# Optimization experiments

Hardware: AMD Instinct MI355X
Metric: run time of the kernel (lower is better)

The kernel has to match this reference:

```python
import jax, jax.numpy as jnp
import numpy as np

B, S, I, H = 128, 256, 512, 512


def setup_inputs() -> dict:
    key = jax.random.key(0)
    ks = jax.random.split(key, 7)
    scale = 1.0 / np.sqrt(H)
    return {
        "x": jax.random.normal(ks[0], (B, S, I), dtype=jnp.float32),
        "hx": jax.random.normal(ks[1], (B, H), dtype=jnp.float32),
        "mask": jax.random.uniform(ks[2], (B, S, 1), dtype=jnp.float32),
        # torch nn.GRUCell params: weight_ih [3H, I], weight_hh [3H, H], biases [3H]
        "W_ih": jax.random.uniform(ks[3], (3 * H, I), minval=-scale, maxval=scale, dtype=jnp.float32),
        "W_hh": jax.random.uniform(ks[4], (3 * H, H), minval=-scale, maxval=scale, dtype=jnp.float32),
        "b_ih": jax.random.uniform(ks[5], (3 * H,), minval=-scale, maxval=scale, dtype=jnp.float32),
        "b_hh": jax.random.uniform(ks[6], (3 * H,), minval=-scale, maxval=scale, dtype=jnp.float32),
    }


def reference(x, hx, mask, W_ih, W_hh, b_ih, b_hh):
    # Precompute input projections for all timesteps in one big GEMM: [B,S,3H]
    gi = jnp.einsum("bsi,gi->bsg", x, W_ih) + b_ih
    gi_s = jnp.moveaxis(gi, 1, 0)      # [S,B,3H]
    mask_s = jnp.moveaxis(mask, 1, 0)  # [S,B,1]

    def step(h, inp):
        gi_t, m_t = inp
        h = h * m_t                                    # masked reset of hidden state
        gh = h @ W_hh.T + b_hh                         # [B,3H]
        i_r, i_z, i_n = jnp.split(gi_t, 3, axis=-1)    # torch gate order: r, z, n
        h_r, h_z, h_n = jnp.split(gh, 3, axis=-1)
        r = jax.nn.sigmoid(i_r + h_r)
        z = jax.nn.sigmoid(i_z + h_z)
        n = jnp.tanh(i_n + r * h_n)
        h_new = (1.0 - z) * n + z * h
        return h_new, h_new

    h_last, hs = jax.lax.scan(step, hx, (gi_s, mask_s))
    return jnp.moveaxis(hs, 0, 1), h_last  # ([B,S,H], [B,H])
```

## Files before the change

kernel.cpp:

```cpp
#include <hip/hip_runtime.h>

typedef __attribute__((ext_vector_type(8))) short bf16x8;
typedef __attribute__((ext_vector_type(4))) float f32x4;
typedef unsigned short ushort_t;
typedef unsigned int uint32;
typedef unsigned long long u64;

#define DEVI __device__ __forceinline__

static constexpr int Bn = 128, Sn = 256, In = 512, Hn = 512;
static constexpr int G3 = 3 * Hn;
static constexpr int GBLK = 32;

static constexpr size_t GI_OFF    = 0;
static constexpr size_t GI_BYTES  = (size_t)Bn * Sn * G3 * 2;
static constexpr size_t WIH_OFF   = GI_OFF + GI_BYTES;
static constexpr size_t WIH_BYTES = (size_t)G3 * In * 2;
static constexpr size_t HBUF_OFF  = WIH_OFF + WIH_BYTES;
static constexpr size_t HBUF_BYTES= (size_t)2 * Bn * Hn * 2;
static constexpr size_t FLAG_OFF  = HBUF_OFF + HBUF_BYTES;
static constexpr size_t FLAG_BYTES= 4096;

DEVI ushort_t f2bf(float f) {
  uint32 u = __builtin_bit_cast(uint32, f);
  u += 0x7FFFu + ((u >> 16) & 1u);
  return (ushort_t)(u >> 16);
}
DEVI float bf2f(ushort_t h) {
  uint32 u = ((uint32)h) << 16;
  return __builtin_bit_cast(float, u);
}
DEVI float sigmoid_f(float x) { return 1.0f / (1.0f + __expf(-x)); }
DEVI float tanh_f(float x)    { return 2.0f / (1.0f + __expf(-2.0f * x)) - 1.0f; }

__global__ void k_cvt_wih(const float* __restrict__ wih, ushort_t* __restrict__ out) {
  int i = blockIdx.x * blockDim.x + threadIdx.x;
  const float4 v = ((const float4*)wih)[i];
  ushort4 o;
  o.x = f2bf(v.x); o.y = f2bf(v.y); o.z = f2bf(v.z); o.w = f2bf(v.w);
  ((ushort4*)out)[i] = o;
}

__launch_bounds__(512)
__global__ void k_gi(const float* __restrict__ x, const ushort_t* __restrict__ wihb,
                     const float* __restrict__ b_ih, ushort_t* __restrict__ gi) {
  extern __shared__ ushort_t apan[];
  const int tid = threadIdx.x;
  const int bm  = blockIdx.x;
#pragma unroll
  for (int it = 0; it < 32; ++it) {
    int fidx = it * 512 + tid;
    int row = fidx >> 7, c4 = fidx & 127;
    const float4 v = *(const float4*)(x + ((size_t)(bm * 128 + row) << 9) + (c4 << 2));
    ushort4 o;
    o.x = f2bf(v.x); o.y = f2bf(v.y); o.z = f2bf(v.z); o.w = f2bf(v.w);
    *(ushort4*)(&apan[row * 520 + (c4 << 2)]) = o;
  }
  __syncthreads();
  const int lane = tid & 63, wid = tid >> 6;
  const int l15 = lane & 15, hi = lane >> 4;
  const int arow = wid * 16 + l15;
  for (int nt = 0; nt < 12; ++nt) {
    const int n0 = nt * 128;
    f32x4 acc[8] = {};
#pragma unroll
    for (int ks = 0; ks < 16; ++ks) {
      bf16x8 a = *(const bf16x8*)(&apan[arow * 520 + ks * 32 + hi * 8]);
#pragma unroll
      for (int j = 0; j < 8; ++j) {
        const ushort_t* wp = wihb + ((size_t)(n0 + j * 16 + l15) << 9) + ks * 32 + hi * 8;
        bf16x8 b = *(const bf16x8*)wp;
        acc[j] = __builtin_amdgcn_mfma_f32_16x16x32_bf16(a, b, acc[j], 0, 0, 0);
      }
    }
#pragma unroll
    for (int j = 0; j < 8; ++j) {
      const int n = n0 + j * 16 + l15;
      const float bias = b_ih[n];
#pragma unroll
      for (int r = 0; r < 4; ++r) {
        int m = bm * 128 + wid * 16 + hi * 4 + r;
        gi[(size_t)m * 1536 + n] = f2bf(acc[j][r] + bias);
      }
    }
  }
}

__launch_bounds__(512)
__global__ void k_scan(const float* __restrict__ hx, const float* __restrict__ mask,
                       const float* __restrict__ whh, const float* __restrict__ bhh,
                       const ushort_t* __restrict__ gi, u64* __restrict__ hbuf,
                       uint32* __restrict__ flags, float* __restrict__ out) {
  __shared__ ushort_t Wl[48 * 520];
  __shared__ ushort_t hpack[128 * 16];
  __shared__ int s_abort;
  const int tid = threadIdx.x;
  const int bid = blockIdx.x;
  const int c0 = bid * 16;
  if (tid == 0) s_abort = 0;

  for (int r = 0; r < 48; ++r) {
    int g = r >> 4, j = r & 15;
    Wl[r * 520 + tid] = f2bf(whh[(size_t)(g * 512 + c0 + j) * 512 + tid]);
  }

  const int lane = tid & 63, wid = tid >> 6;
  const int l15 = lane & 15, hi = lane >> 4;
  const int arow = wid * 16 + l15;

  float hreg[4];
#pragma unroll
  for (int r = 0; r < 4; ++r) {
    int b = wid * 16 + hi * 4 + r;
    hreg[r] = hx[b * 512 + c0 + l15] * mask[b * 256];
    hpack[b * 16 + l15] = f2bf(hreg[r]);
  }
  __syncthreads();
  {
    int b = tid >> 2, q = tid & 3;
    u64 v = *(const u64*)(&hpack[b * 16 + q * 4]);
    __hip_atomic_store(hbuf + (size_t)b * 128 + (c0 >> 2) + q, v,
                       __ATOMIC_RELAXED, __HIP_MEMORY_SCOPE_AGENT);
  }

  ushort_t pg0[4], pg1[4], pg2[4];
  float pmk[4];
#pragma unroll
  for (int r = 0; r < 4; ++r) {
    int b = wid * 16 + hi * 4 + r;
    size_t gb = (size_t)(b * 256 + 0) * 1536 + c0 + l15;
    pg0[r] = gi[gb];
    pg1[r] = gi[gb + 512];
    pg2[r] = gi[gb + 1024];
    pmk[r] = mask[b * 256 + 1];
  }

  __syncthreads();
  if (s_abort == 0) {
    if (tid == 0)
      __hip_atomic_store(flags + bid * 32, 1u, __ATOMIC_RELAXED,
                         __HIP_MEMORY_SCOPE_AGENT);
    if (tid < 32) {
      int ok = 0;
      for (int spin = 0; spin < 50000; ++spin) {
        if (__hip_atomic_load(flags + tid * 32, __ATOMIC_RELAXED,
                              __HIP_MEMORY_SCOPE_AGENT) >= 1u) { ok = 1; break; }
        __builtin_amdgcn_s_sleep(1);
      }
      if (!ok) s_abort = 1;
    }
  }
  __syncthreads();

  const float bhh_r = bhh[c0 + l15];
  const float bhh_z = bhh[512 + c0 + l15];
  const float bhh_n = bhh[1024 + c0 + l15];
  int p = 0;

  for (int t = 0; t < 256; ++t) {
    const u64* hb = hbuf + (size_t)p * (128 * 128);
    u64 ha[32];
#pragma unroll
    for (int ks = 0; ks < 16; ++ks) {
      size_t base = (size_t)arow * 128 + ks * 8 + hi * 2;
      ha[2 * ks]     = __hip_atomic_load(hb + base, __ATOMIC_RELAXED, __HIP_MEMORY_SCOPE_AGENT);
      ha[2 * ks + 1] = __hip_atomic_load(hb + base + 1, __ATOMIC_RELAXED, __HIP_MEMORY_SCOPE_AGENT);
    }
    __builtin_amdgcn_sched_barrier(0);

    f32x4 acc[3] = {};
#pragma unroll
    for (int ks = 0; ks < 16; ++ks) {
      union { u64 q[2]; bf16x8 v; } ua;
      ua.q[0] = ha[2 * ks]; ua.q[1] = ha[2 * ks + 1];
#pragma unroll
      for (int g = 0; g < 3; ++g) {
        bf16x8 w = *(const bf16x8*)(&Wl[(g * 16 + l15) * 520 + ks * 32 + hi * 8]);
        acc[g] = __builtin_amdgcn_mfma_f32_16x16x32_bf16(ua.v, w, acc[g], 0, 0, 0);
      }
    }

#pragma unroll
    for (int r = 0; r < 4; ++r) {
      int b = wid * 16 + hi * 4 + r;
      float rg = sigmoid_f(bf2f(pg0[r]) + acc[0][r] + bhh_r);
      float zg = sigmoid_f(bf2f(pg1[r]) + acc[1][r] + bhh_z);
      float ng = tanh_f(bf2f(pg2[r]) + rg * (acc[2][r] + bhh_n));
      float hn = (1.0f - zg) * ng + zg * hreg[r];
      out[(size_t)(b * 256 + t) * 512 + c0 + l15] = hn;
      if (t == 255) {
        out[(size_t)(128 * 256) * 512 + b * 512 + c0 + l15] = hn;
      } else {
        float hm = hn * pmk[r];
        hreg[r] = hm;
        hpack[b * 16 + l15] = f2bf(hm);
      }
    }

    if (t < 255) {
      __syncthreads();
      {
        int b = tid >> 2, q = tid & 3;
        u64 v = *(const u64*)(&hpack[b * 16 + q * 4]);
        __hip_atomic_store(hbuf + (size_t)(p ^ 1) * (128 * 128) + (size_t)b * 128 + (c0 >> 2) + q,
                           v, __ATOMIC_RELAXED, __HIP_MEMORY_SCOPE_AGENT);
      }
      __syncthreads();
      if (s_abort == 0) {
        if (tid == 0)
          __hip_atomic_store(flags + bid * 32, (uint32)(t + 2), __ATOMIC_RELAXED,
                             __HIP_MEMORY_SCOPE_AGENT);
      }
      {
        int tn = t + 1;
#pragma unroll
        for (int r = 0; r < 4; ++r) {
          int b = wid * 16 + hi * 4 + r;
          size_t gb = (size_t)(b * 256 + tn) * 1536 + c0 + l15;
          pg0[r] = gi[gb];
          pg1[r] = gi[gb + 512];
          pg2[r] = gi[gb + 1024];
          pmk[r] = (tn < 255) ? mask[b * 256 + tn + 1] : 0.0f;
        }
      }
      if (s_abort == 0) {
        if (tid < 32) {
          uint32 want = (uint32)(t + 2);
          int ok = 0;
          for (int spin = 0; spin < 50000; ++spin) {
            if (__hip_atomic_load(flags + tid * 32, __ATOMIC_RELAXED,
                                  __HIP_MEMORY_SCOPE_AGENT) >= want) { ok = 1; break; }
            __builtin_amdgcn_s_sleep(1);
          }
          if (!ok) s_abort = 1;
        }
      }
      __syncthreads();
      p ^= 1;
    }
  }
}

extern "C" void kernel_launch(void* const* d_in, const int* in_sizes, int n_in,
                              void* d_out, int out_size, void* d_ws, size_t ws_size,
                              hipStream_t stream) {
  (void)in_sizes; (void)n_in; (void)out_size; (void)ws_size;
  const float* x    = (const float*)d_in[0];
  const float* hx   = (const float*)d_in[1];
  const float* mask = (const float*)d_in[2];
  const float* Wih  = (const float*)d_in[3];
  const float* Whh  = (const float*)d_in[4];
  const float* bih  = (const float*)d_in[5];
  const float* bhh  = (const float*)d_in[6];
  float* out = (float*)d_out;
  char* ws = (char*)d_ws;
  ushort_t* gi    = (ushort_t*)(ws + GI_OFF);
  ushort_t* wihb  = (ushort_t*)(ws + WIH_OFF);
  u64*      hbuf  = (u64*)(ws + HBUF_OFF);
  uint32*   flags = (uint32*)(ws + FLAG_OFF);

  hipMemsetAsync(flags, 0, FLAG_BYTES, stream);
  k_cvt_wih<<<768, 256, 0, stream>>>(Wih, wihb);
  k_gi<<<256, 512, 128 * 520 * 2, stream>>>(x, wihb, bih, gi);
  k_scan<<<GBLK, 512, 0, stream>>>(hx, mask, Whh, bhh, gi, hbuf, flags, out);
}
```

Measured before the change: 2.771 ms.

## Place scan workgroups on a single XCD and sync through shared L2 with sc0

Launches 256 workgroups, has each record its XCC_ID, and keeps 32 blocks that share one XCD, so the recurrent scan runs within one L2 domain. Those blocks exchange the hidden state and step flags with sc0 loads and stores plus an L1 invalidate, replacing agent-scope atomics, so each per-step exchange should stay in local L2 instead of going through cross-die coherence. A verification handshake falls back to the old atomic path if the fast handshake fails. Risks are relying on undocumented placement and cache-coherence behaviour, and extra launch overhead from the idle blocks.

```diff
diff --git a/kernel.cpp b/kernel.cpp
--- a/kernel.cpp
+++ b/kernel.cpp
@@ -10,16 +10,17 @@
 
 static constexpr int Bn = 128, Sn = 256, In = 512, Hn = 512;
 static constexpr int G3 = 3 * Hn;
-static constexpr int GBLK = 32;
 
 static constexpr size_t GI_OFF    = 0;
 static constexpr size_t GI_BYTES  = (size_t)Bn * Sn * G3 * 2;
 static constexpr size_t WIH_OFF   = GI_OFF + GI_BYTES;
 static constexpr size_t WIH_BYTES = (size_t)G3 * In * 2;
-static constexpr size_t HBUF_OFF  = WIH_OFF + WIH_BYTES;
-static constexpr size_t HBUF_BYTES= (size_t)2 * Bn * Hn * 2;
-static constexpr size_t FLAG_OFF  = HBUF_OFF + HBUF_BYTES;
-static constexpr size_t FLAG_BYTES= 4096;
+static constexpr size_t HBUFF_OFF = WIH_OFF + WIH_BYTES;
+static constexpr size_t HBUFM_OFF = HBUFF_OFF + 262144;
+static constexpr size_t FLAGF_OFF = HBUFM_OFF + 262144;
+static constexpr size_t FLAGM_OFF = FLAGF_OFF + 4096;
+static constexpr size_t VERD_OFF  = FLAGM_OFF + 4096;
+static constexpr size_t ARR_OFF   = VERD_OFF + 4096;
 
 DEVI ushort_t f2bf(float f) {
   uint32 u = __builtin_bit_cast(uint32, f);
@@ -32,6 +33,7 @@
 }
 DEVI float sigmoid_f(float x) { return 1.0f / (1.0f + __expf(-x)); }
 DEVI float tanh_f(float x)    { return 2.0f / (1.0f + __expf(-2.0f * x)) - 1.0f; }
+DEVI void l1_inv() { asm volatile("buffer_inv sc0" ::: "memory"); }
 
 __global__ void k_cvt_wih(const float* __restrict__ wih, ushort_t* __restrict__ out) {
   int i = blockIdx.x * blockDim.x + threadIdx.x;
@@ -87,17 +89,54 @@
 }
 
 __launch_bounds__(512)
-__global__ void k_scan(const float* __restrict__ hx, const float* __restrict__ mask,
-                       const float* __restrict__ whh, const float* __restrict__ bhh,
-                       const ushort_t* __restrict__ gi, u64* __restrict__ hbuf,
-                       uint32* __restrict__ flags, float* __restrict__ out) {
+__global__ void k_scan3(const float* __restrict__ hx, const float* __restrict__ mask,
+                        const float* __restrict__ whh, const float* __restrict__ bhh,
+                        const ushort_t* __restrict__ gi,
+                        u64* __restrict__ hbufF, u64* __restrict__ hbufM,
+                        uint32* __restrict__ flagF, uint32* __restrict__ flagM,
+                        uint32* __restrict__ verd, uint32* __restrict__ arr,
+                        float* __restrict__ out) {
   __shared__ ushort_t Wl[48 * 520];
   __shared__ ushort_t hpack[128 * 16];
+  __shared__ unsigned char xl[256];
+  __shared__ int meta[2];
   __shared__ int s_abort;
   const int tid = threadIdx.x;
   const int bid = blockIdx.x;
-  const int c0 = bid * 16;
-  if (tid == 0) s_abort = 0;
+
+  uint32 xcd;
+  asm("s_getreg_b32 %0, hwreg(HW_REG_XCC_ID)" : "=s"(xcd));
+  if (tid == 0) {
+    s_abort = 0;
+    __hip_atomic_store(&arr[bid], 0x80u | xcd, __ATOMIC_RELAXED, __HIP_MEMORY_SCOPE_AGENT);
+  }
+  const int widx = tid & 255;
+  uint32 aval = 0;
+  int ok = 0;
+  for (int spin = 0; spin < 20000 && !ok; ++spin) {
+    aval = __hip_atomic_load(&arr[widx], __ATOMIC_RELAXED, __HIP_MEMORY_SCOPE_AGENT);
+    ok = __syncthreads_and((int)(aval & 0x80u));
+    if (!ok) __builtin_amdgcn_s_sleep(8);
+  }
+  if (!ok) return;
+  xl[widx] = (unsigned char)(aval & 0x7fu);
+  __syncthreads();
+  if (tid == 0) {
+    int cnt[16] = {};
+    int rank = 0;
+    for (int j = 0; j < 256; ++j) {
+      int x = xl[j] & 15;
+      cnt[x]++;
+      if (j < bid && x == (int)(xcd & 15)) rank++;
+    }
+    int wr = -1;
+    for (int x = 0; x < 16; ++x) if (cnt[x] >= 32) { wr = x; break; }
+    meta[0] = rank; meta[1] = wr;
+  }
+  __syncthreads();
+  const int rank = meta[0], wr = meta[1];
+  if (wr < 0 || (int)(xcd & 15) != wr || rank >= 32) return;
+  const int c0 = rank * 16;
 
   for (int r = 0; r < 48; ++r) {
     int g = r >> 4, j = r & 15;
@@ -116,11 +155,63 @@
     hpack[b * 16 + l15] = f2bf(hreg[r]);
   }
   __syncthreads();
+
   {
     int b = tid >> 2, q = tid & 3;
     u64 v = *(const u64*)(&hpack[b * 16 + q * 4]);
-    __hip_atomic_store(hbuf + (size_t)b * 128 + (c0 >> 2) + q, v,
-                       __ATOMIC_RELAXED, __HIP_MEMORY_SCOPE_AGENT);
+    u64* dst = hbufF + (size_t)b * 128 + (c0 >> 2) + q;
+    asm volatile("global_store_dwordx2 %0, %1, off sc0" :: "v"(dst), "v"(v) : "memory");
+  }
+  __syncthreads();
+  if (tid == 0) {
+    uint32 one = 1;
+    asm volatile("global_store_dword %0, %1, off sc0" :: "v"(flagF + rank * 32), "v"(one) : "memory");
+  }
+  int got = 0;
+  if (tid < 32) {
+    for (int spin = 0; spin < 5000; ++spin) {
+      l1_inv();
+      uint32 f;
+      asm volatile("global_load_dword %0, %1, off sc0\n\ts_waitcnt vmcnt(0)"
+                   : "=v"(f) : "v"(flagF + tid * 32) : "memory");
+      if (f >= 1u) { got = 1; break; }
+      __builtin_amdgcn_s_sleep(1);
+    }
+  }
+  int fastmode = __syncthreads_and((tid < 32) ? got : 1);
+  if (tid == 0)
+    __hip_atomic_store(verd + rank * 32, fastmode ? 1u : 2u, __ATOMIC_RELAXED, __HIP_MEMORY_SCOPE_AGENT);
+  uint32 pv = 0;
+  if (tid < 32) {
+    for (int spin = 0; spin < 50000; ++spin) {
+      pv = __hip_atomic_load(verd + tid * 32, __ATOMIC_RELAXED, __HIP_MEMORY_SCOPE_AGENT);
+      if (pv) break;
+      __builtin_amdgcn_s_sleep(1);
+    }
+  }
+  int present = __syncthreads_and((tid < 32) ? (pv != 0) : 1);
+  if (!present) return;
+  fastmode = __syncthreads_and((tid < 32) ? (pv == 1u) : 1);
+
+  if (!fastmode) {
+    {
+      int b = tid >> 2, q = tid & 3;
+      u64 v = *(const u64*)(&hpack[b * 16 + q * 4]);
+      __hip_atomic_store(hbufM + (size_t)b * 128 + (c0 >> 2) + q, v,
+                         __ATOMIC_RELAXED, __HIP_MEMORY_SCOPE_AGENT);
+    }
+    __syncthreads();
+    if (tid == 0)
+      __hip_atomic_store(flagM + rank * 32, 1u, __ATOMIC_RELAXED, __HIP_MEMORY_SCOPE_AGENT);
+    int g2 = 0;
+    if (tid < 32) {
+      for (int spin = 0; spin < 50000; ++spin) {
+        if (__hip_atomic_load(flagM + tid * 32, __ATOMIC_RELAXED, __HIP_MEMORY_SCOPE_AGENT) >= 1u) { g2 = 1; break; }
+        __builtin_amdgcn_s_sleep(1);
+      }
+      if (!g2) s_abort = 1;
+    }
+    __syncthreads();
   }
 
   ushort_t pg0[4], pg1[4], pg2[4];
@@ -135,38 +226,34 @@
     pmk[r] = mask[b * 256 + 1];
   }
 
-  __syncthreads();
-  if (s_abort == 0) {
-    if (tid == 0)
-      __hip_atomic_store(flags + bid * 32, 1u, __ATOMIC_RELAXED,
-                         __HIP_MEMORY_SCOPE_AGENT);
-    if (tid < 32) {
-      int ok = 0;
-      for (int spin = 0; spin < 50000; ++spin) {
-        if (__hip_atomic_load(flags + tid * 32, __ATOMIC_RELAXED,
-                              __HIP_MEMORY_SCOPE_AGENT) >= 1u) { ok = 1; break; }
-        __builtin_amdgcn_s_sleep(1);
-      }
-      if (!ok) s_abort = 1;
-    }
-  }
-  __syncthreads();
-
   const float bhh_r = bhh[c0 + l15];
   const float bhh_z = bhh[512 + c0 + l15];
   const float bhh_n = bhh[1024 + c0 + l15];
   int p = 0;
 
   for (int t = 0; t < 256; ++t) {
-    const u64* hb = hbuf + (size_t)p * (128 * 128);
     u64 ha[32];
-#pragma unroll
-    for (int ks = 0; ks < 16; ++ks) {
-      size_t base = (size_t)arow * 128 + ks * 8 + hi * 2;
-      ha[2 * ks]     = __hip_atomic_load(hb + base, __ATOMIC_RELAXED, __HIP_MEMORY_SCOPE_AGENT);
-      ha[2 * ks + 1] = __hip_atomic_load(hb + base + 1, __ATOMIC_RELAXED, __HIP_MEMORY_SCOPE_AGENT);
-    }
-    __builtin_amdgcn_sched_barrier(0);
+    if (fastmode) {
+      const u64* hb = hbufF + (size_t)p * 16384;
+      l1_inv();
+#pragma unroll
+      for (int ks = 0; ks < 16; ++ks) {
+        const u64* ap = hb + (size_t)arow * 128 + ks * 8 + hi * 2;
+        asm volatile("global_load_dwordx2 %0, %1, off sc0" : "=v"(ha[2 * ks]) : "v"(ap));
+        asm volatile("global_load_dwordx2 %0, %1, off sc0" : "=v"(ha[2 * ks + 1]) : "v"(ap + 1));
+      }
+      asm volatile("s_waitcnt vmcnt(0)" ::: "memory");
+      __builtin_amdgcn_sched_barrier(0);
+    } else {
+      const u64* hb = hbufM + (size_t)p * 16384;
+#pragma unroll
+      for (int ks = 0; ks < 16; ++ks) {
+        size_t base = (size_t)arow * 128 + ks * 8 + hi * 2;
+        ha[2 * ks]     = __hip_atomic_load(hb + base, __ATOMIC_RELAXED, __HIP_MEMORY_SCOPE_AGENT);
+        ha[2 * ks + 1] = __hip_atomic_load(hb + base + 1, __ATOMIC_RELAXED, __HIP_MEMORY_SCOPE_AGENT);
+      }
+      __builtin_amdgcn_sched_barrier(0);
+    }
 
     f32x4 acc[3] = {};
 #pragma unroll
@@ -202,14 +289,22 @@
       {
         int b = tid >> 2, q = tid & 3;
         u64 v = *(const u64*)(&hpack[b * 16 + q * 4]);
-        __hip_atomic_store(hbuf + (size_t)(p ^ 1) * (128 * 128) + (size_t)b * 128 + (c0 >> 2) + q,
-                           v, __ATOMIC_RELAXED, __HIP_MEMORY_SCOPE_AGENT);
+        size_t off = (size_t)(p ^ 1) * 16384 + (size_t)b * 128 + (c0 >> 2) + q;
+        if (fastmode) {
+          u64* dst = hbufF + off;
+          asm volatile("global_store_dwordx2 %0, %1, off sc0" :: "v"(dst), "v"(v) : "memory");
+        } else {
+          __hip_atomic_store(hbufM + off, v, __ATOMIC_RELAXED, __HIP_MEMORY_SCOPE_AGENT);
+        }
       }
       __syncthreads();
-      if (s_abort == 0) {
-        if (tid == 0)
-          __hip_atomic_store(flags + bid * 32, (uint32)(t + 2), __ATOMIC_RELAXED,
-                             __HIP_MEMORY_SCOPE_AGENT);
+      if (!s_abort && tid == 0) {
+        uint32 want = (uint32)(t + 2);
+        if (fastmode) {
+          asm volatile("global_store_dword %0, %1, off sc0" :: "v"(flagF + rank * 32), "v"(want) : "memory");
+        } else {
+          __hip_atomic_store(flagM + rank * 32, want, __ATOMIC_RELAXED, __HIP_MEMORY_SCOPE_AGENT);
+        }
       }
       {
         int tn = t + 1;
@@ -223,17 +318,22 @@
           pmk[r] = (tn < 255) ? mask[b * 256 + tn + 1] : 0.0f;
         }
       }
-      if (s_abort == 0) {
-        if (tid < 32) {
-          uint32 want = (uint32)(t + 2);
-          int ok = 0;
-          for (int spin = 0; spin < 50000; ++spin) {
-            if (__hip_atomic_load(flags + tid * 32, __ATOMIC_RELAXED,
-                                  __HIP_MEMORY_SCOPE_AGENT) >= want) { ok = 1; break; }
-            __builtin_amdgcn_s_sleep(1);
+      if (!s_abort && tid < 32) {
+        uint32 want = (uint32)(t + 2);
+        int g3 = 0;
+        for (int spin = 0; spin < 50000; ++spin) {
+          uint32 f;
+          if (fastmode) {
+            l1_inv();
+            asm volatile("global_load_dword %0, %1, off sc0\n\ts_waitcnt vmcnt(0)"
+                         : "=v"(f) : "v"(flagF + tid * 32) : "memory");
+          } else {
+            f = __hip_atomic_load(flagM + tid * 32, __ATOMIC_RELAXED, __HIP_MEMORY_SCOPE_AGENT);
           }
-          if (!ok) s_abort = 1;
+          if (f >= want) { g3 = 1; break; }
+          __builtin_amdgcn_s_sleep(1);
         }
+        if (!g3) s_abort = 1;
       }
       __syncthreads();
       p ^= 1;
@@ -256,11 +356,16 @@
   char* ws = (char*)d_ws;
   ushort_t* gi    = (ushort_t*)(ws + GI_OFF);
   ushort_t* wihb  = (ushort_t*)(ws + WIH_OFF);
-  u64*      hbuf  = (u64*)(ws + HBUF_OFF);
-  uint32*   flags = (uint32*)(ws + FLAG_OFF);
-
-  hipMemsetAsync(flags, 0, FLAG_BYTES, stream);
+  u64*      hbufF = (u64*)(ws + HBUFF_OFF);
+  u64*      hbufM = (u64*)(ws + HBUFM_OFF);
+  uint32*   flagF = (uint32*)(ws + FLAGF_OFF);
+  uint32*   flagM = (uint32*)(ws + FLAGM_OFF);
+  uint32*   verd  = (uint32*)(ws + VERD_OFF);
+  uint32*   arr   = (uint32*)(ws + ARR_OFF);
+
+  hipMemsetAsync(ws + FLAGF_OFF, 0, 4096 * 3 + 1024, stream);
   k_cvt_wih<<<768, 256, 0, stream>>>(Wih, wihb);
   k_gi<<<256, 512, 128 * 520 * 2, stream>>>(x, wihb, bih, gi);
-  k_scan<<<GBLK, 512, 0, stream>>>(hx, mask, Whh, bhh, gi, hbuf, flags, out);
-}
+  k_scan3<<<256, 512, 0, stream>>>(hx, mask, Whh, bhh, gi, hbufF, hbufM,
+                                   flagF, flagM, verd, arr, out);
+}
```

Result: slower. 3.486 ms (+25.8%).

## Replace block barriers with per-wave flag sync and cache-bypassing inline-asm loads

Applied to the files above, without the earlier changes.

The recurrent scan drops its per-step __syncthreads barriers and LDS staging of h. Each wave now writes its bf16 hidden slice straight to global memory and raises its own per-wave flag. A lane-parallel __all poll over all 32x8 flags replaces the single-thread spin, and the sleep only starts after 64 spins. On paths that pass a startup probe handshake, loads and stores use inline asm with sc0 sc1 bits to get coherent access at lower cost than the atomics. This shortens the critical path of the global step-to-step barrier, at the cost of extra startup protocol complexity and reliance on hand-written memory-coherence asm.

```diff
diff --git a/kernel.cpp b/kernel.cpp
--- a/kernel.cpp
+++ b/kernel.cpp
@@ -8,18 +8,15 @@
 
 #define DEVI __device__ __forceinline__
 
-static constexpr int Bn = 128, Sn = 256, In = 512, Hn = 512;
-static constexpr int G3 = 3 * Hn;
-static constexpr int GBLK = 32;
-
 static constexpr size_t GI_OFF    = 0;
-static constexpr size_t GI_BYTES  = (size_t)Bn * Sn * G3 * 2;
+static constexpr size_t GI_BYTES  = (size_t)128 * 256 * 1536 * 2;
 static constexpr size_t WIH_OFF   = GI_OFF + GI_BYTES;
-static constexpr size_t WIH_BYTES = (size_t)G3 * In * 2;
+static constexpr size_t WIH_BYTES = (size_t)1536 * 512 * 2;
 static constexpr size_t HBUF_OFF  = WIH_OFF + WIH_BYTES;
-static constexpr size_t HBUF_BYTES= (size_t)2 * Bn * Hn * 2;
-static constexpr size_t FLAG_OFF  = HBUF_OFF + HBUF_BYTES;
-static constexpr size_t FLAG_BYTES= 4096;
+static constexpr size_t FLAG_OFF  = HBUF_OFF + 262144;
+static constexpr size_t PRB_OFF   = FLAG_OFF + 4096;
+static constexpr size_t PFLG_OFF  = PRB_OFF + 4096;
+static constexpr size_t VERD_OFF  = PFLG_OFF + 4096;
 
 DEVI ushort_t f2bf(float f) {
   uint32 u = __builtin_bit_cast(uint32, f);
@@ -32,6 +29,43 @@
 }
 DEVI float sigmoid_f(float x) { return 1.0f / (1.0f + __expf(-x)); }
 DEVI float tanh_f(float x)    { return 2.0f / (1.0f + __expf(-2.0f * x)) - 1.0f; }
+
+DEVI void sc_store32(uint32* p, uint32 v) {
+  asm volatile("global_store_dword %0, %1, off sc0 sc1" :: "v"(p), "v"(v) : "memory");
+}
+DEVI uint32 sc_load32(const uint32* p) {
+  uint32 v;
+  asm volatile("global_load_dword %0, %1, off sc0 sc1\n\ts_waitcnt vmcnt(0)"
+               : "=v"(v) : "v"(p) : "memory");
+  return v;
+}
+DEVI void sc_store16(ushort_t* p, uint32 v) {
+  asm volatile("global_store_short %0, %1, off sc0 sc1" :: "v"(p), "v"(v) : "memory");
+}
+DEVI void vm0() { asm volatile("s_waitcnt vmcnt(0)" ::: "memory"); }
+
+template<bool FAST> DEVI void hst(ushort_t* p, ushort_t v) {
+  if (FAST) sc_store16(p, (uint32)v);
+  else __hip_atomic_store(p, v, __ATOMIC_RELAXED, __HIP_MEMORY_SCOPE_AGENT);
+}
+template<bool FAST> DEVI void fst(uint32* p, uint32 v) {
+  if (FAST) sc_store32(p, v);
+  else __hip_atomic_store(p, v, __ATOMIC_RELAXED, __HIP_MEMORY_SCOPE_AGENT);
+}
+template<bool FAST> DEVI uint32 fld(const uint32* p) {
+  if (FAST) return sc_load32(p);
+  return __hip_atomic_load(p, __ATOMIC_RELAXED, __HIP_MEMORY_SCOPE_AGENT);
+}
+
+template<bool FAST>
+DEVI int pollring(const uint32* flags, int lane, int wid, uint32 want, int cap) {
+  for (int spin = 0; spin < cap; ++spin) {
+    uint32 f = fld<FAST>(flags + (size_t)(lane & 31) * 32 + wid);
+    if (__all((int)(f >= want))) return 1;
+    if (spin >= 64) __builtin_amdgcn_s_sleep(1);
+  }
+  return 0;
+}
 
 __global__ void k_cvt_wih(const float* __restrict__ wih, ushort_t* __restrict__ out) {
   int i = blockIdx.x * blockDim.x + threadIdx.x;
@@ -86,85 +120,62 @@
   }
 }
 
-__launch_bounds__(512)
-__global__ void k_scan(const float* __restrict__ hx, const float* __restrict__ mask,
-                       const float* __restrict__ whh, const float* __restrict__ bhh,
-                       const ushort_t* __restrict__ gi, u64* __restrict__ hbuf,
-                       uint32* __restrict__ flags, float* __restrict__ out) {
-  __shared__ ushort_t Wl[48 * 520];
-  __shared__ ushort_t hpack[128 * 16];
-  __shared__ int s_abort;
-  const int tid = threadIdx.x;
-  const int bid = blockIdx.x;
-  const int c0 = bid * 16;
-  if (tid == 0) s_abort = 0;
-
-  for (int r = 0; r < 48; ++r) {
-    int g = r >> 4, j = r & 15;
-    Wl[r * 520 + tid] = f2bf(whh[(size_t)(g * 512 + c0 + j) * 512 + tid]);
-  }
-
+template<bool FAST>
+DEVI void scan_run(const float* __restrict__ hx, const ushort_t* __restrict__ gi,
+                   const float* __restrict__ mask, const float* __restrict__ bhh,
+                   const ushort_t* Wl, u64* __restrict__ hbuf,
+                   uint32* __restrict__ flags, float* __restrict__ out,
+                   int rank, int tid) {
   const int lane = tid & 63, wid = tid >> 6;
   const int l15 = lane & 15, hi = lane >> 4;
+  const int c0 = rank * 16;
   const int arow = wid * 16 + l15;
+  ushort_t* hbs = (ushort_t*)hbuf;
 
   float hreg[4];
 #pragma unroll
   for (int r = 0; r < 4; ++r) {
     int b = wid * 16 + hi * 4 + r;
     hreg[r] = hx[b * 512 + c0 + l15] * mask[b * 256];
-    hpack[b * 16 + l15] = f2bf(hreg[r]);
-  }
-  __syncthreads();
-  {
-    int b = tid >> 2, q = tid & 3;
-    u64 v = *(const u64*)(&hpack[b * 16 + q * 4]);
-    __hip_atomic_store(hbuf + (size_t)b * 128 + (c0 >> 2) + q, v,
-                       __ATOMIC_RELAXED, __HIP_MEMORY_SCOPE_AGENT);
-  }
-
+    hst<FAST>(hbs + (size_t)b * 512 + c0 + l15, f2bf(hreg[r]));
+  }
   ushort_t pg0[4], pg1[4], pg2[4];
   float pmk[4];
 #pragma unroll
   for (int r = 0; r < 4; ++r) {
     int b = wid * 16 + hi * 4 + r;
-    size_t gb = (size_t)(b * 256 + 0) * 1536 + c0 + l15;
-    pg0[r] = gi[gb];
-    pg1[r] = gi[gb + 512];
-    pg2[r] = gi[gb + 1024];
+    size_t gb = (size_t)(b * 256) * 1536 + c0 + l15;
+    pg0[r] = gi[gb]; pg1[r] = gi[gb + 512]; pg2[r] = gi[gb + 1024];
     pmk[r] = mask[b * 256 + 1];
   }
-
-  __syncthreads();
-  if (s_abort == 0) {
-    if (tid == 0)
-      __hip_atomic_store(flags + bid * 32, 1u, __ATOMIC_RELAXED,
-                         __HIP_MEMORY_SCOPE_AGENT);
-    if (tid < 32) {
-      int ok = 0;
-      for (int spin = 0; spin < 50000; ++spin) {
-        if (__hip_atomic_load(flags + tid * 32, __ATOMIC_RELAXED,
-                              __HIP_MEMORY_SCOPE_AGENT) >= 1u) { ok = 1; break; }
-        __builtin_amdgcn_s_sleep(1);
-      }
-      if (!ok) s_abort = 1;
-    }
-  }
-  __syncthreads();
-
-  const float bhh_r = bhh[c0 + l15];
-  const float bhh_z = bhh[512 + c0 + l15];
-  const float bhh_n = bhh[1024 + c0 + l15];
+  vm0();
+  if (lane == 0) fst<FAST>(flags + rank * 32 + wid, 1u);
+  int nopoll = !pollring<FAST>(flags, lane, wid, 1u, 200000);
+
+  const float bhr = bhh[c0 + l15];
+  const float bhz = bhh[512 + c0 + l15];
+  const float bhn = bhh[1024 + c0 + l15];
   int p = 0;
 
   for (int t = 0; t < 256; ++t) {
-    const u64* hb = hbuf + (size_t)p * (128 * 128);
     u64 ha[32];
-#pragma unroll
-    for (int ks = 0; ks < 16; ++ks) {
-      size_t base = (size_t)arow * 128 + ks * 8 + hi * 2;
-      ha[2 * ks]     = __hip_atomic_load(hb + base, __ATOMIC_RELAXED, __HIP_MEMORY_SCOPE_AGENT);
-      ha[2 * ks + 1] = __hip_atomic_load(hb + base + 1, __ATOMIC_RELAXED, __HIP_MEMORY_SCOPE_AGENT);
+    if (FAST) {
+      const u64* hbb = hbuf + (size_t)p * 16384 + (size_t)arow * 128 + hi * 2;
+#pragma unroll
+      for (int ks = 0; ks < 16; ++ks) {
+        asm volatile("global_load_dwordx2 %0, %1, off offset:%2 sc0 sc1"
+                     : "=v"(ha[2 * ks]) : "v"(hbb), "i"(ks * 64) : "memory");
+        asm volatile("global_load_dwordx2 %0, %1, off offset:%2 sc0 sc1"
+                     : "=v"(ha[2 * ks + 1]) : "v"(hbb), "i"(ks * 64 + 8) : "memory");
+      }
+      vm0();
+    } else {
+      const u64* hbb = hbuf + (size_t)p * 16384 + (size_t)arow * 128 + hi * 2;
+#pragma unroll
+      for (int ks = 0; ks < 16; ++ks) {
+        ha[2 * ks]     = __hip_atomic_load(hbb + ks * 8, __ATOMIC_RELAXED, __HIP_MEMORY_SCOPE_AGENT);
+        ha[2 * ks + 1] = __hip_atomic_load(hbb + ks * 8 + 1, __ATOMIC_RELAXED, __HIP_MEMORY_SCOPE_AGENT);
+      }
     }
     __builtin_amdgcn_sched_barrier(0);
 
@@ -180,65 +191,126 @@
       }
     }
 
+    float hn[4];
+#pragma unroll
+    for (int r = 0; r < 4; ++r) {
+      float rg = sigmoid_f(bf2f(pg0[r]) + acc[0][r] + bhr);
+      float zg = sigmoid_f(bf2f(pg1[r]) + acc[1][r] + bhz);
+      float ng = tanh_f(bf2f(pg2[r]) + rg * (acc[2][r] + bhn));
+      hn[r] = (1.0f - zg) * ng + zg * hreg[r];
+    }
+
+    if (t < 255) {
+      ushort_t* hw = hbs + (size_t)(p ^ 1) * 65536;
+#pragma unroll
+      for (int r = 0; r < 4; ++r) {
+        int b = wid * 16 + hi * 4 + r;
+        float hm = hn[r] * pmk[r];
+        hreg[r] = hm;
+        hst<FAST>(hw + (size_t)b * 512 + c0 + l15, f2bf(hm));
+      }
+      vm0();
+      if (lane == 0) fst<FAST>(flags + rank * 32 + wid, (uint32)(t + 2));
+    }
+
 #pragma unroll
     for (int r = 0; r < 4; ++r) {
       int b = wid * 16 + hi * 4 + r;
-      float rg = sigmoid_f(bf2f(pg0[r]) + acc[0][r] + bhh_r);
-      float zg = sigmoid_f(bf2f(pg1[r]) + acc[1][r] + bhh_z);
-      float ng = tanh_f(bf2f(pg2[r]) + rg * (acc[2][r] + bhh_n));
-      float hn = (1.0f - zg) * ng + zg * hreg[r];
-      out[(size_t)(b * 256 + t) * 512 + c0 + l15] = hn;
-      if (t == 255) {
-        out[(size_t)(128 * 256) * 512 + b * 512 + c0 + l15] = hn;
-      } else {
-        float hm = hn * pmk[r];
-        hreg[r] = hm;
-        hpack[b * 16 + l15] = f2bf(hm);
-      }
-    }
-
+      out[(size_t)(b * 256 + t) * 512 + c0 + l15] = hn[r];
+      if (t == 255)
+        out[(size_t)(128 * 256) * 512 + b * 512 + c0 + l15] = hn[r];
+    }
     if (t < 255) {
-      __syncthreads();
-      {
-        int b = tid >> 2, q = tid & 3;
-        u64 v = *(const u64*)(&hpack[b * 16 + q * 4]);
-        __hip_atomic_store(hbuf + (size_t)(p ^ 1) * (128 * 128) + (size_t)b * 128 + (c0 >> 2) + q,
-                           v, __ATOMIC_RELAXED, __HIP_MEMORY_SCOPE_AGENT);
-      }
-      __syncthreads();
-      if (s_abort == 0) {
-        if (tid == 0)
-          __hip_atomic_store(flags + bid * 32, (uint32)(t + 2), __ATOMIC_RELAXED,
-                             __HIP_MEMORY_SCOPE_AGENT);
-      }
-      {
-        int tn = t + 1;
-#pragma unroll
-        for (int r = 0; r < 4; ++r) {
-          int b = wid * 16 + hi * 4 + r;
-          size_t gb = (size_t)(b * 256 + tn) * 1536 + c0 + l15;
-          pg0[r] = gi[gb];
-          pg1[r] = gi[gb + 512];
-          pg2[r] = gi[gb + 1024];
-          pmk[r] = (tn < 255) ? mask[b * 256 + tn + 1] : 0.0f;
-        }
-      }
-      if (s_abort == 0) {
-        if (tid < 32) {
-          uint32 want = (uint32)(t + 2);
-          int ok = 0;
-          for (int spin = 0; spin < 50000; ++spin) {
-            if (__hip_atomic_load(flags + tid * 32, __ATOMIC_RELAXED,
-                                  __HIP_MEMORY_SCOPE_AGENT) >= want) { ok = 1; break; }
-            __builtin_amdgcn_s_sleep(1);
-          }
-          if (!ok) s_abort = 1;
-        }
-      }
-      __syncthreads();
+      int tn = t + 1;
+#pragma unroll
+      for (int r = 0; r < 4; ++r) {
+        int b = wid * 16 + hi * 4 + r;
+        size_t gb = (size_t)(b * 256 + tn) * 1536 + c0 + l15;
+        pg0[r] = gi[gb]; pg1[r] = gi[gb + 512]; pg2[r] = gi[gb + 1024];
+        pmk[r] = (tn < 255) ? mask[b * 256 + tn + 1] : 0.0f;
+      }
+      if (!nopoll)
+        nopoll = !pollring<FAST>(flags, lane, wid, (uint32)(t + 2), 20000);
       p ^= 1;
     }
   }
+}
+
+__launch_bounds__(512)
+__global__ void k_scan5(const float* __restrict__ hx, const float* __restrict__ mask,
+                        const float* __restrict__ whh, const float* __restrict__ bhh,
+                        const ushort_t* __restrict__ gi, u64* __restrict__ hbuf,
+                        uint32* __restrict__ flags, uint32* __restrict__ prb,
+                        uint32* __restrict__ pflg, uint32* __restrict__ verd,
+                        float* __restrict__ out) {
+  __shared__ ushort_t Wl[48 * 520];
+  const int tid = threadIdx.x;
+  const int rank = blockIdx.x;
+
+  for (int r = 0; r < 48; ++r) {
+    int g = r >> 4, j = r & 15;
+    Wl[r * 520 + tid] = f2bf(whh[(size_t)(g * 512 + rank * 16 + j) * 512 + tid]);
+  }
+
+  int okp = 1;
+  if (tid == 0) {
+    sc_store32(prb + rank * 32, 0xA5000000u | (uint32)rank);
+    vm0();
+    sc_store32(pflg + rank * 32, 1u);
+  }
+  if (tid < 32) {
+    int got = 0;
+    for (int spin = 0; spin < 200000; ++spin) {
+      if (sc_load32(pflg + tid * 32) >= 1u) { got = 1; break; }
+      if (spin >= 64) __builtin_amdgcn_s_sleep(1);
+    }
+    okp = got && (sc_load32(prb + tid * 32) == (0xA5000000u | (uint32)tid));
+  }
+  __syncthreads();
+  if (tid == 0) sc_store32(pflg + rank * 32, 2u);
+  if (tid < 32 && okp) {
+    int got = 0;
+    for (int spin = 0; spin < 50000; ++spin) {
+      if (sc_load32(pflg + tid * 32) >= 2u) { got = 1; break; }
+      if (spin >= 64) __builtin_amdgcn_s_sleep(1);
+    }
+    okp = got;
+  }
+  __syncthreads();
+  if (tid == 0) {
+    sc_store32(prb + rank * 32, 0x5A000000u | (uint32)rank);
+    vm0();
+    sc_store32(pflg + rank * 32, 3u);
+  }
+  if (tid < 32 && okp) {
+    int got = 0;
+    for (int spin = 0; spin < 50000; ++spin) {
+      if (sc_load32(pflg + tid * 32) >= 3u) { got = 1; break; }
+      if (spin >= 64) __builtin_amdgcn_s_sleep(1);
+    }
+    okp = got && (sc_load32(prb + tid * 32) == (0x5A000000u | (uint32)tid));
+  }
+  int myfast = __syncthreads_and((tid < 32) ? okp : 1);
+
+  if (tid == 0)
+    __hip_atomic_store(verd + rank * 32, myfast ? 1u : 2u, __ATOMIC_RELAXED,
+                       __HIP_MEMORY_SCOPE_AGENT);
+  uint32 pv = 0;
+  if (tid < 32) {
+    for (int spin = 0; spin < 200000; ++spin) {
+      pv = __hip_atomic_load(verd + tid * 32, __ATOMIC_RELAXED, __HIP_MEMORY_SCOPE_AGENT);
+      if (pv) break;
+      if (spin >= 64) __builtin_amdgcn_s_sleep(1);
+    }
+  }
+  int present = __syncthreads_and((tid < 32) ? (pv != 0) : 1);
+  if (!present) return;
+  int fastmode = __syncthreads_and((tid < 32) ? (pv == 1u) : 1);
+
+  if (fastmode)
+    scan_run<true >(hx, gi, mask, bhh, Wl, hbuf, flags, out, rank, tid);
+  else
+    scan_run<false>(hx, gi, mask, bhh, Wl, hbuf, flags, out, rank, tid);
 }
 
 extern "C" void kernel_launch(void* const* d_in, const int* in_sizes, int n_in,
@@ -258,9 +330,13 @@
   ushort_t* wihb  = (ushort_t*)(ws + WIH_OFF);
   u64*      hbuf  = (u64*)(ws + HBUF_OFF);
   uint32*   flags = (uint32*)(ws + FLAG_OFF);
-
-  hipMemsetAsync(flags, 0, FLAG_BYTES, stream);
+  uint32*   prb   = (uint32*)(ws + PRB_OFF);
+  uint32*   pflg  = (uint32*)(ws + PFLG_OFF);
+  uint32*   verd  = (uint32*)(ws + VERD_OFF);
+
+  hipMemsetAsync(ws + FLAG_OFF, 0, 4096 * 4, stream);
   k_cvt_wih<<<768, 256, 0, stream>>>(Wih, wihb);
   k_gi<<<256, 512, 128 * 520 * 2, stream>>>(x, wihb, bih, gi);
-  k_scan<<<GBLK, 512, 0, stream>>>(hx, mask, Whh, bhh, gi, hbuf, flags, out);
-}
+  k_scan5<<<32, 512, 0, stream>>>(hx, mask, Whh, bhh, gi, hbuf,
+                                  flags, prb, pflg, verd, out);
+}
```

New measurement: 3.082 ms. +11.2%, slower.
